# Kernel tuning notes

Hardware: AMD Instinct MI355X
Metric: run time of the kernel (lower is better)

## Reference

```python
import jax, jax.numpy as jnp
import numpy as np

ALPHA = 4.0  # spikingjelly default Sigmoid surrogate alpha
BN_EPS = 1e-5

@jax.custom_vjp
def _spike(v):
    return (v >= 0.0).astype(v.dtype)

def _spike_fwd(v):
    return _spike(v), v

def _spike_bwd(v, g):
    s = jax.nn.sigmoid(ALPHA * v)
    return (g * ALPHA * s * (1.0 - s),)

_spike.defvjp(_spike_fwd, _spike_bwd)

def lif(x, v_th):
    # Single-step LIFNode(tau=2, v_reset=0) starting from v=0:
    # v = v + (x - v)/tau = x/2 ; spike = Heaviside(v - v_th)
    return _spike(x * 0.5 - v_th)

def bn(x, p):
    # p: [4, C] = gamma, beta, running_mean, running_var (inference BN)
    g, b, m, v = p
    scale = g * jax.lax.rsqrt(v + BN_EPS)
    return x * scale[None, :, None, None] + (b - m * scale)[None, :, None, None]

def conv1x1(x, w):
    # x: [B,C,H,W], w: [O,C]
    return jnp.einsum('bchw,oc->bohw', x, w)

def dwconv3x3(x, w):
    # depthwise 3x3, w: [C,3,3]
    C = x.shape[1]
    return jax.lax.conv_general_dilated(
        x, w[:, None], (1, 1), 'SAME',
        feature_group_count=C,
        dimension_numbers=('NCHW', 'OIHW', 'NCHW'))

def branch(x, w1, dw, w2, bns):
    # RepConv: conv1x1 -> BN -> (dw3x3 -> pw1x1 -> BN), then the extra Sequential BN
    x = bn(conv1x1(x, w1), bns[0])
    x = bn(conv1x1(dwconv3x3(x, dw), w2), bns[1])
    return bn(x, bns[2])

def setup_inputs() -> dict:
    key = jax.random.key(0)
    ks = jax.random.split(key, 5)
    B, C, H, W = 16, 256, 80, 80
    x = jax.random.normal(ks[0], (B, C, H, W), jnp.float32) * 2.0  # so LIFs actually fire
    w1 = jax.random.normal(ks[1], (4, C, C), jnp.float32) * 0.06
    dw = jax.random.normal(ks[2], (4, C, 3, 3), jnp.float32) * 0.3
    w2 = jax.random.normal(ks[3], (4, C, C), jnp.float32) * 0.06
    bn_params = jax.random.uniform(ks[4], (4, 3, 4, C), jnp.float32, 0.1, 1.0)
    return {"x": x, "w1": w1, "dw": dw, "w2": w2, "bn_params": bn_params}

def reference(x, w1, dw, w2, bn_params):
    scale = 0.125
    xs = lif(x, 1.0)                                   # head_lif
    q = branch(xs, w1[0], dw[0], w2[0], bn_params[0])  # q_conv (q_lif unused in source)
    k = branch(xs, w1[1], dw[1], w2[1], bn_params[1])  # k_conv (k_lif unused in source)
    v = branch(xs, w1[2], dw[2], w2[2], bn_params[2])  # v_conv
    v = lif(v, 1.0)                                    # v_lif -> binary spikes
    # k.transpose(-2,-1) @ v : per (b,c) [W,H] @ [H,W] -> [W,W]
    kv = jnp.einsum('bchw,bchu->bcwu', k, v)
    # q @ kv : [H,W] @ [W,W] -> [H,W]
    attn = jnp.einsum('bchw,bcwu->bchu', q, kv) * scale
    s = lif(attn, 0.5)                                 # attn_lif, v_threshold=0.5
    return branch(s, w1[3], dw[3], w2[3], bn_params[3])  # proj_conv
```

## Files before the change

### kernel.cpp

```cpp
#include <hip/hip_runtime.h>
#include <hip/hip_bf16.h>
#include <cstdint>
#include <cstddef>
#include <cmath>

typedef unsigned short u16;
typedef unsigned char  u8;
typedef unsigned int   u32;
typedef __attribute__((ext_vector_type(8))) short short8;
typedef __attribute__((ext_vector_type(4))) float f32x4;
typedef __attribute__((ext_vector_type(4))) u16 u16x4;

#define CCH 256
#define HWP 6400

__device__ __forceinline__ u16 f2bf(float f) {
  u32 u = __float_as_uint(f);
  u = (u + 0x7FFFu + ((u >> 16) & 1u)) >> 16;
  return (u16)u;
}
__device__ __forceinline__ float bf2f(u16 h) { return __uint_as_float(((u32)h) << 16); }
__device__ __forceinline__ void split3(float v, u16& h, u16& m, u16& l) {
  h = f2bf(v); float r = v - bf2f(h);
  m = f2bf(r); l = f2bf(r - bf2f(m));
}
__device__ __forceinline__ void gl_lds16(const void* g, void* l) {
  __builtin_amdgcn_global_load_lds((const __attribute__((address_space(1))) unsigned int*)g,
                                   (__attribute__((address_space(3))) unsigned int*)l,
                                   16, 0, 0);
}

__global__ __launch_bounds__(256) void fold_weights(
    const float* __restrict__ w1, const float* __restrict__ w2,
    const float* __restrict__ bnp,
    u16* __restrict__ w1h, u16* __restrict__ w1m, u16* __restrict__ w1l,
    u16* __restrict__ w2h, u16* __restrict__ w2m, u16* __restrict__ w2l,
    float* __restrict__ b0f, float* __restrict__ b2f)
{
  int i = blockIdx.x >> 8, o = blockIdx.x & 255, c = threadIdx.x;
  const float* bp = bnp + i * 3072;
  double g0 = bp[0 + o],    be0 = bp[256 + o],  m0 = bp[512 + o],  v0 = bp[768 + o];
  double g1 = bp[1024 + o], be1 = bp[1280 + o], m1 = bp[1536 + o], v1 = bp[1792 + o];
  double g2 = bp[2048 + o], be2 = bp[2304 + o], m2 = bp[2560 + o], v2 = bp[2816 + o];
  double s0 = g0 / sqrt(v0 + 1e-5);
  double s1 = g1 / sqrt(v1 + 1e-5);
  double s2 = g2 / sqrt(v2 + 1e-5);
  size_t ro = (size_t)(i * 256 + o) * 256;
  float wa = (float)(s0 * (double)w1[ro + c]);
  float wb = (float)(s1 * s2 * (double)w2[ro + c]);
  u16 h, m, l;
  split3(wa, h, m, l); w1h[ro + c] = h; w1m[ro + c] = m; w1l[ro + c] = l;
  split3(wb, h, m, l); w2h[ro + c] = h; w2m[ro + c] = m; w2l[ro + c] = l;
  if (c == 0) {
    b0f[i * 256 + o] = (float)(be0 - m0 * s0);
    b2f[i * 256 + o] = (float)(s2 * (be1 - m1 * s1) + be2 - m2 * s2);
  }
}

__global__ __launch_bounds__(256) void head_spike(
    const float* __restrict__ x, u8* __restrict__ xs, int b0)
{
  __shared__ u8 tile[64][68];
  int z = blockIdx.z, c0 = blockIdx.y << 6, p0 = blockIdx.x << 6;
  int tid = threadIdx.x;
  const float* xb = x + ((size_t)(b0 + z) * CCH + c0) * HWP + p0;
#pragma unroll
  for (int j = 0; j < 16; ++j) {
    int idx = j * 256 + tid;
    int cl = idx >> 6, pl = idx & 63;
    tile[pl][cl] = (xb[(size_t)cl * HWP + pl] >= 2.0f) ? 1 : 0;
  }
  __syncthreads();
#pragma unroll
  for (int j = 0; j < 4; ++j) {
    int idx = j * 256 + tid;
    int row = idx >> 4, c4 = (idx & 15) << 2;
    *(uchar4*)(xs + ((size_t)z * HWP + p0 + row) * CCH + c0 + c4) =
        *(const uchar4*)&tile[row][c4];
  }
}

__global__ __launch_bounds__(256) void transpose_s(
    const u8* __restrict__ in, u8* __restrict__ out, int b0)
{
  __shared__ u8 tile[64][68];
  int z = blockIdx.z, c0 = blockIdx.y << 6, p0 = blockIdx.x << 6;
  int tid = threadIdx.x;
#pragma unroll
  for (int j = 0; j < 4; ++j) {
    int idx = j * 256 + tid;
    int cl = idx >> 4, p4 = (idx & 15) << 2;
    uchar4 v = *(const uchar4*)(in + ((size_t)z * CCH + c0 + cl) * HWP + p0 + p4);
    tile[p4 + 0][cl] = v.x; tile[p4 + 1][cl] = v.y;
    tile[p4 + 2][cl] = v.z; tile[p4 + 3][cl] = v.w;
  }
  __syncthreads();
#pragma unroll
  for (int j = 0; j < 4; ++j) {
    int idx = j * 256 + tid;
    int row = idx >> 4, c4 = (idx & 15) << 2;
    *(uchar4*)(out + ((size_t)(b0 + z) * HWP + p0 + row) * CCH + c0 + c4) =
        *(const uchar4*)&tile[row][c4];
  }
}

__global__ __launch_bounds__(256) void gemm1(
    const u8* __restrict__ act, int b0in,
    const u16* __restrict__ WH, const u16* __restrict__ WM, const u16* __restrict__ WL,
    const float* __restrict__ bias, float* __restrict__ T1)
{
  __shared__ alignas(16) u16 As[128 * 40];
  __shared__ alignas(16) u16 LWH[4096];
  __shared__ alignas(16) u16 LWM[4096];
  __shared__ alignas(16) u16 LWL[4096];
  const int tid = threadIdx.x, wave = tid >> 6, lane = tid & 63;
  const int p0 = blockIdx.x * 128, o0 = blockIdx.y * 128, z = blockIdx.z;
  const int wm = (wave >> 1) * 64, wn = (wave & 1) * 64;
  const int lc = lane & 15, lr = lane >> 4;
  const u8* ab = act + ((size_t)(b0in + z) * HWP + p0) * CCH;
  const char* whb = (const char*)(WH + (size_t)o0 * 256);
  const char* wmb = (const char*)(WM + (size_t)o0 * 256);
  const char* wlb = (const char*)(WL + (size_t)o0 * 256);

  f32x4 acc[4][4];
#pragma unroll
  for (int i = 0; i < 4; ++i)
#pragma unroll
    for (int j = 0; j < 4; ++j) acc[i][j] = (f32x4){0.f, 0.f, 0.f, 0.f};

  const int srow = tid >> 1, shalf = tid & 1;

  for (int kc = 0; kc < 8; ++kc) {
    const int kof = kc * 64;
    __syncthreads();
#pragma unroll
    for (int t = 0; t < 2; ++t) {
      int li = t * 256 + tid;
      int row = li >> 2, ch = li & 3;
      int chp = (ch - row - (row >> 2)) & 3;
      size_t so = (size_t)row * 512 + kof + chp * 16;
      int base = (t * 256 + wave * 64) * 8;
      gl_lds16(whb + so, &LWH[base]);
      gl_lds16(wmb + so, &LWM[base]);
      gl_lds16(wlb + so, &LWL[base]);
    }
    uint4 u = *(const uint4*)(ab + (size_t)srow * CCH + kc * 32 + shalf * 16);
    u32 vv[4] = {u.x, u.y, u.z, u.w};
    u32 w[8];
#pragma unroll
    for (int q = 0; q < 4; ++q) {
      u32 v = vv[q];
      w[2 * q]     = ((v & 255u) ? 0x3F80u : 0u) | (((v >> 8) & 255u) ? 0x3F800000u : 0u);
      w[2 * q + 1] = (((v >> 16) & 255u) ? 0x3F80u : 0u) | (((v >> 24) & 255u) ? 0x3F800000u : 0u);
    }
    *(uint4*)&As[srow * 40 + shalf * 16]     = (uint4){w[0], w[1], w[2], w[3]};
    *(uint4*)&As[srow * 40 + shalf * 16 + 8] = (uint4){w[4], w[5], w[6], w[7]};
    __syncthreads();
    short8 af[4];
#pragma unroll
    for (int i = 0; i < 4; ++i)
      af[i] = *(const short8*)&As[(wm + i * 16 + lc) * 40 + lr * 8];
#pragma unroll
    for (int j = 0; j < 4; ++j) {
      int row = wn + j * 16 + lc;
      int o = row * 32 + ((lr + lc + (lc >> 2)) & 3) * 8;
      short8 bh = *(const short8*)&LWH[o];
      short8 bm = *(const short8*)&LWM[o];
      short8 bl = *(const short8*)&LWL[o];
#pragma unroll
      for (int i = 0; i < 4; ++i) {
        acc[i][j] = __builtin_amdgcn_mfma_f32_16x16x32_bf16(af[i], bl, acc[i][j], 0, 0, 0);
        acc[i][j] = __builtin_amdgcn_mfma_f32_16x16x32_bf16(af[i], bm, acc[i][j], 0, 0, 0);
        acc[i][j] = __builtin_amdgcn_mfma_f32_16x16x32_bf16(af[i], bh, acc[i][j], 0, 0, 0);
      }
    }
  }
  float* tb = T1 + ((size_t)z * HWP + p0) * CCH + o0;
#pragma unroll
  for (int j = 0; j < 4; ++j) {
    int n = wn + j * 16 + lc;
    float bn_ = bias[o0 + n];
#pragma unroll
    for (int i = 0; i < 4; ++i) {
      int m = wm + i * 16 + lr * 4;
#pragma unroll
      for (int r = 0; r < 4; ++r)
        tb[(size_t)(m + r) * CCH + n] = acc[i][j][r] + bn_;
    }
  }
}

__global__ __launch_bounds__(256) void dw3(
    const float* __restrict__ t1, const float* __restrict__ dwk,
    u16* __restrict__ oh, u16* __restrict__ om, u16* __restrict__ ol)
{
  __shared__ float wl[2304];
  int tid = threadIdx.x;
#pragma unroll
  for (int t = 0; t < 9; ++t) wl[t * 256 + tid] = dwk[t * 256 + tid];
  int c4 = (tid & 63) << 2;
  int pl = tid >> 6;
  int p = blockIdx.x * 4 + pl;
  int z = blockIdx.y;
  int y = p / 80, x = p - y * 80;
  __syncthreads();
  float a0 = 0.f, a1 = 0.f, a2 = 0.f, a3 = 0.f;
  const float* base = t1 + (size_t)z * HWP * CCH;
  const float* wc = &wl[c4 * 9];
#pragma unroll
  for (int dy = -1; dy <= 1; ++dy) {
    int yy = y + dy;
    bool vy = (unsigned)yy < 80u;
#pragma unroll
    for (int dx = -1; dx <= 1; ++dx) {
      int xx = x + dx;
      if (vy && (unsigned)xx < 80u) {
        float4 v = *(const float4*)(base + (size_t)(yy * 80 + xx) * CCH + c4);
        int t = (dy + 1) * 3 + (dx + 1);
        a0 += wc[t]      * v.x;
        a1 += wc[9 + t]  * v.y;
        a2 += wc[18 + t] * v.z;
        a3 += wc[27 + t] * v.w;
      }
    }
  }
  u16 h0, m0, l0, h1, m1, l1, h2, m2, l2, h3, m3, l3;
  split3(a0, h0, m0, l0);
  split3(a1, h1, m1, l1);
  split3(a2, h2, m2, l2);
  split3(a3, h3, m3, l3);
  u16x4 vh, vm, vlo;
  vh.x = h0; vh.y = h1; vh.z = h2; vh.w = h3;
  vm.x = m0; vm.y = m1; vm.z = m2; vm.w = m3;
  vlo.x = l0; vlo.y = l1; vlo.z = l2; vlo.w = l3;
  size_t addr = ((size_t)z * HWP + p) * CCH + c4;
  *(u16x4*)(oh + addr) = vh;
  *(u16x4*)(om + addr) = vm;
  *(u16x4*)(ol + addr) = vlo;
}

template <int MODE>
__global__ __launch_bounds__(256) void gemm2s(
    const u16* __restrict__ AH, const u16* __restrict__ AM, const u16* __restrict__ AL,
    const u16* __restrict__ WH, const u16* __restrict__ WM, const u16* __restrict__ WL,
    const float* __restrict__ bias, int b0,
    float* __restrict__ outF, u8* __restrict__ outB)
{
  __shared__ alignas(16) u16 LAH[4096];
  __shared__ alignas(16) u16 LAM[4096];
  __shared__ alignas(16) u16 LAL[4096];
  __shared__ alignas(16) u16 LWH[4096];
  __shared__ alignas(16) u16 LWM[4096];
  __shared__ alignas(16) u16 LWL[4096];
  const int tid = threadIdx.x, wave = tid >> 6, lane = tid & 63;
  const int p0 = blockIdx.x * 128, o0 = blockIdx.y * 128, z = blockIdx.z;
  const int wm = (wave >> 1) * 64, wn = (wave & 1) * 64;
  const int lc = lane & 15, lr = lane >> 4;
  const char* ahb = (const char*)(AH + ((size_t)z * HWP + p0) * 256);
  const char* amb = (const char*)(AM + ((size_t)z * HWP + p0) * 256);
  const char* alb = (const char*)(AL + ((size_t)z * HWP + p0) * 256);
  const char* whb = (const char*)(WH + (size_t)o0 * 256);
  const char* wmb = (const char*)(WM + (size_t)o0 * 256);
  const char* wlb = (const char*)(WL + (size_t)o0 * 256);

  f32x4 acc[4][4];
#pragma unroll
  for (int i = 0; i < 4; ++i)
#pragma unroll
    for (int j = 0; j < 4; ++j) acc[i][j] = (f32x4){0.f, 0.f, 0.f, 0.f};

  for (int kc = 0; kc < 8; ++kc) {
    const int kof = kc * 64;
#pragma unroll
    for (int t = 0; t < 2; ++t) {
      int li = t * 256 + tid;
      int row = li >> 2, ch = li & 3;
      int chp = (ch - row - (row >> 2)) & 3;
      size_t so = (size_t)row * 512 + kof + chp * 16;
      int base = (t * 256 + wave * 64) * 8;
      gl_lds16(ahb + so, &LAH[base]);
      gl_lds16(amb + so, &LAM[base]);
      gl_lds16(alb + so, &LAL[base]);
      gl_lds16(whb + so, &LWH[base]);
      gl_lds16(wmb + so, &LWM[base]);
      gl_lds16(wlb + so, &LWL[base]);
    }
    __syncthreads();
    short8 afH[4], afM[4], afL[4];
#pragma unroll
    for (int i = 0; i < 4; ++i) {
      int row = wm + i * 16 + lc;
      int o = row * 32 + ((lr + lc + (lc >> 2)) & 3) * 8;
      afH[i] = *(const short8*)&LAH[o];
      afM[i] = *(const short8*)&LAM[o];
      afL[i] = *(const short8*)&LAL[o];
    }
#pragma unroll
    for (int j = 0; j < 4; ++j) {
      int row = wn + j * 16 + lc;
      int o = row * 32 + ((lr + lc + (lc >> 2)) & 3) * 8;
      short8 bh = *(const short8*)&LWH[o];
      short8 bm = *(const short8*)&LWM[o];
      short8 bl = *(const short8*)&LWL[o];
#pragma unroll
      for (int i = 0; i < 4; ++i) {
        acc[i][j] = __builtin_amdgcn_mfma_f32_16x16x32_bf16(afM[i], bm, acc[i][j], 0, 0, 0);
        acc[i][j] = __builtin_amdgcn_mfma_f32_16x16x32_bf16(afL[i], bh, acc[i][j], 0, 0, 0);
        acc[i][j] = __builtin_amdgcn_mfma_f32_16x16x32_bf16(afH[i], bl, acc[i][j], 0, 0, 0);
        acc[i][j] = __builtin_amdgcn_mfma_f32_16x16x32_bf16(afM[i], bh, acc[i][j], 0, 0, 0);
        acc[i][j] = __builtin_amdgcn_mfma_f32_16x16x32_bf16(afH[i], bm, acc[i][j], 0, 0, 0);
        acc[i][j] = __builtin_amdgcn_mfma_f32_16x16x32_bf16(afH[i], bh, acc[i][j], 0, 0, 0);
      }
    }
    __syncthreads();
  }
#pragma unroll
  for (int j = 0; j < 4; ++j) {
    int n = o0 + wn + j * 16 + lc;
    float bn_ = bias[n];
    size_t rowb = ((size_t)(b0 + z) * CCH + n) * HWP + p0;
#pragma unroll
    for (int i = 0; i < 4; ++i) {
      int m = wm + i * 16 + lr * 4;
      if (MODE == 0) {
        float4 o;
        o.x = acc[i][j][0] + bn_; o.y = acc[i][j][1] + bn_;
        o.z = acc[i][j][2] + bn_; o.w = acc[i][j][3] + bn_;
        *(float4*)(outF + rowb + m) = o;
      } else {
        uchar4 o;
        o.x = (acc[i][j][0] + bn_ >= 2.0f) ? 1 : 0;
        o.y = (acc[i][j][1] + bn_ >= 2.0f) ? 1 : 0;
        o.z = (acc[i][j][2] + bn_ >= 2.0f) ? 1 : 0;
        o.w = (acc[i][j][3] + bn_ >= 2.0f) ? 1 : 0;
        *(uchar4*)(outB + rowb + m) = o;
      }
    }
  }
}

__global__ __launch_bounds__(320) void attn_k(
    const float* __restrict__ qf, const float* __restrict__ kf,
    const u8* __restrict__ vv, u8* __restrict__ s)
{
  __shared__ alignas(16) u16 L[24960];
  __shared__ alignas(16) u8  VT[8320];
  const int tid = threadIdx.x, wave = tid >> 6, lane = tid & 63;
  const int lc = lane & 15, lr = lane >> 4;
  const size_t off = (size_t)blockIdx.x * HWP;
  u16* KH = L; u16* KM = L + 8320; u16* KL = L + 16640;

  for (int t = 0; t < 12; ++t) {
    int i = t * 320 + tid;
    if (i < 3840) {
      int pl = i / 1280, rem = i - pl * 1280;
      L[pl * 8320 + (rem >> 4) * 104 + 80 + (rem & 15)] = 0;
    }
  }
  for (int t = 0; t < 4; ++t) {
    int i = t * 320 + tid;
    if (i < 1280) VT[(i >> 4) * 104 + 80 + (i & 15)] = 0;
  }
  for (int t = 0; t < 20; ++t) {
    int idx = t * 320 + tid;
    int h = idx / 80, w = idx - h * 80;
    u16 hh, mm, ll; split3(kf[off + idx], hh, mm, ll);
    KH[h * 104 + w] = hh; KM[h * 104 + w] = mm; KL[h * 104 + w] = ll;
    VT[w * 104 + h] = vv[off + idx];
  }
  __syncthreads();

  f32x4 accS[5];
#pragma unroll
  for (int n = 0; n < 5; ++n) accS[n] = (f32x4){0.f, 0.f, 0.f, 0.f};
  const int hrow = wave * 16 + lc;
  for (int kc = 0; kc < 3; ++kc) {
    short8 qh, qm, ql;
    int w0 = kc * 32 + lr * 8;
    if (w0 < 80) {
      const float* qp = qf + off + hrow * 80 + w0;
      float4 a = *(const float4*)qp;
      float4 b = *(const float4*)(qp + 4);
      float qv[8] = {a.x, a.y, a.z, a.w, b.x, b.y, b.z, b.w};
#pragma unroll
      for (int e = 0; e < 8; ++e) {
        u16 hh, mm, ll; split3(qv[e], hh, mm, ll);
        qh[e] = (short)hh; qm[e] = (short)mm; ql[e] = (short)ll;
      }
    } else {
      qh = (short8){0,0,0,0,0,0,0,0}; qm = qh; ql = qh;
    }
#pragma unroll
    for (int n = 0; n < 5; ++n) {
      int bo = (n * 16 + lc) * 104 + kc * 32 + lr * 8;
      short8 kh_ = *(const short8*)&KH[bo];
      short8 km_ = *(const short8*)&KM[bo];
      short8 kl_ = *(const short8*)&KL[bo];
      accS[n] = __builtin_amdgcn_mfma_f32_16x16x32_bf16(qh, kl_, accS[n], 0, 0, 0);
      accS[n] = __builtin_amdgcn_mfma_f32_16x16x32_bf16(ql, kh_, accS[n], 0, 0, 0);
      accS[n] = __builtin_amdgcn_mfma_f32_16x16x32_bf16(qm, km_, accS[n], 0, 0, 0);
      accS[n] = __builtin_amdgcn_mfma_f32_16x16x32_bf16(qm, kh_, accS[n], 0, 0, 0);
      accS[n] = __builtin_amdgcn_mfma_f32_16x16x32_bf16(qh, km_, accS[n], 0, 0, 0);
      accS[n] = __builtin_amdgcn_mfma_f32_16x16x32_bf16(qh, kh_, accS[n], 0, 0, 0);
    }
  }
  __syncthreads();
  for (int t = 0; t < 12; ++t) {
    int i = t * 320 + tid;
    if (i < 3840) {
      int pl = i / 1280, rem = i - pl * 1280;
      L[pl * 8320 + (rem >> 4) * 104 + 80 + (rem & 15)] = 0;
    }
  }
#pragma unroll
  for (int n = 0; n < 5; ++n) {
#pragma unroll
    for (int r = 0; r < 4; ++r) {
      u16 hh, mm, ll; split3(accS[n][r], hh, mm, ll);
      int o = (wave * 16 + lr * 4 + r) * 104 + n * 16 + lc;
      KH[o] = hh; KM[o] = mm; KL[o] = ll;
    }
  }
  __syncthreads();
  f32x4 accA[5];
#pragma unroll
  for (int n = 0; n < 5; ++n) accA[n] = (f32x4){0.f, 0.f, 0.f, 0.f};
  for (int kc = 0; kc < 3; ++kc) {
    int ao = (wave * 16 + lc) * 104 + kc * 32 + lr * 8;
    short8 sh_ = *(const short8*)&KH[ao];
    short8 sm_ = *(const short8*)&KM[ao];
    short8 sl_ = *(const short8*)&KL[ao];
#pragma unroll
    for (int n = 0; n < 5; ++n) {
      const u8* vp = &VT[(n * 16 + lc) * 104 + kc * 32 + lr * 8];
      u32 b0 = *(const u32*)vp;
      u32 b1 = *(const u32*)(vp + 4);
      u32 e0 = ((b0 & 255u) ? 0x3F80u : 0u) | (((b0 >> 8) & 255u) ? 0x3F800000u : 0u);
      u32 e1 = (((b0 >> 16) & 255u) ? 0x3F80u : 0u) | (((b0 >> 24) & 255u) ? 0x3F800000u : 0u);
      u32 e2 = ((b1 & 255u) ? 0x3F80u : 0u) | (((b1 >> 8) & 255u) ? 0x3F800000u : 0u);
      u32 e3 = (((b1 >> 16) & 255u) ? 0x3F80u : 0u) | (((b1 >> 24) & 255u) ? 0x3F800000u : 0u);
      u32 vbw[4] = {e0, e1, e2, e3};
      short8 vb = *(const short8*)vbw;
      accA[n] = __builtin_amdgcn_mfma_f32_16x16x32_bf16(sl_, vb, accA[n], 0, 0, 0);
      accA[n] = __builtin_amdgcn_mfma_f32_16x16x32_bf16(sm_, vb, accA[n], 0, 0, 0);
      accA[n] = __builtin_amdgcn_mfma_f32_16x16x32_bf16(sh_, vb, accA[n], 0, 0, 0);
    }
  }
#pragma unroll
  for (int n = 0; n < 5; ++n)
#pragma unroll
    for (int r = 0; r < 4; ++r)
      s[off + (size_t)(wave * 16 + lr * 4 + r) * 80 + n * 16 + lc] =
          (accA[n][r] >= 8.0f) ? 1 : 0;
}

extern "C" void kernel_launch(void* const* d_in, const int* in_sizes, int n_in,
                              void* d_out, int out_size, void* d_ws, size_t ws_size,
                              hipStream_t stream)
{
  const float* x   = (const float*)d_in[0];
  const float* w1  = (const float*)d_in[1];
  const float* dwk = (const float*)d_in[2];
  const float* w2  = (const float*)d_in[3];
  const float* bnp = (const float*)d_in[4];
  float* out = (float*)d_out;
  char* ws = (char*)d_ws;

  u16* W1H = (u16*)(ws + 0);
  u16* W1M = (u16*)(ws + 524288);
  u16* W1L = (u16*)(ws + 1048576);
  u16* W2H = (u16*)(ws + 1572864);
  u16* W2M = (u16*)(ws + 2097152);
  u16* W2L = (u16*)(ws + 2621440);
  float* B0F = (float*)(ws + 3145728);
  float* B2F = (float*)(ws + 3149824);
  u8*    SPM = (u8*)(ws + 3153920);
  u8*    XS  = (u8*)(ws + 29368320);
  float* T1  = (float*)(ws + 42475520);
  float* QF  = (float*)(ws + 94904320);
  float* KF  = (float*)(ws + 147333120);
  u8*    V   = (u8*)(ws + 199761920);
  u16*   D2H = (u16*)(ws + 212869120);
  u16*   D2M = (u16*)(ws + 239083520);
  u16*   D2L = (u16*)(ws + 265297920);

  dim3 gb(256);
  fold_weights<<<dim3(1024), gb, 0, stream>>>(w1, w2, bnp,
      W1H, W1M, W1L, W2H, W2M, W2L, B0F, B2F);

  for (int c = 0; c < 2; ++c) {
    int b0 = c * 8;
    dim3 gh(100, 4, 8), gg(50, 2, 8), gd(1600, 8);
    head_spike<<<gh, gb, 0, stream>>>(x, XS, b0);
    gemm1<<<gg, gb, 0, stream>>>(XS, 0, W1H + 0 * 65536, W1M + 0 * 65536, W1L + 0 * 65536,
                                 B0F + 0, T1);
    dw3<<<gd, gb, 0, stream>>>(T1, dwk + 0 * 2304, D2H, D2M, D2L);
    gemm2s<0><<<gg, gb, 0, stream>>>(D2H, D2M, D2L,
                                     W2H + 0 * 65536, W2M + 0 * 65536, W2L + 0 * 65536,
                                     B2F + 0, 0, QF, nullptr);
    gemm1<<<gg, gb, 0, stream>>>(XS, 0, W1H + 1 * 65536, W1M + 1 * 65536, W1L + 1 * 65536,
                                 B0F + 256, T1);
    dw3<<<gd, gb, 0, stream>>>(T1, dwk + 1 * 2304, D2H, D2M, D2L);
    gemm2s<0><<<gg, gb, 0, stream>>>(D2H, D2M, D2L,
                                     W2H + 1 * 65536, W2M + 1 * 65536, W2L + 1 * 65536,
                                     B2F + 256, 0, KF, nullptr);
    gemm1<<<gg, gb, 0, stream>>>(XS, 0, W1H + 2 * 65536, W1M + 2 * 65536, W1L + 2 * 65536,
                                 B0F + 512, T1);
    dw3<<<gd, gb, 0, stream>>>(T1, dwk + 2 * 2304, D2H, D2M, D2L);
    gemm2s<1><<<gg, gb, 0, stream>>>(D2H, D2M, D2L,
                                     W2H + 2 * 65536, W2M + 2 * 65536, W2L + 2 * 65536,
                                     B2F + 512, 0, nullptr, V);
    attn_k<<<dim3(2048), dim3(320), 0, stream>>>(QF, KF, V, V);
    transpose_s<<<gh, gb, 0, stream>>>(V, SPM, b0);
  }
  for (int c = 0; c < 2; ++c) {
    int b0 = c * 8;
    dim3 gg(50, 2, 8), gd(1600, 8);
    gemm1<<<gg, gb, 0, stream>>>(SPM, b0, W1H + 3 * 65536, W1M + 3 * 65536, W1L + 3 * 65536,
                                 B0F + 768, T1);
    dw3<<<gd, gb, 0, stream>>>(T1, dwk + 3 * 2304, D2H, D2M, D2L);
    gemm2s<0><<<gg, gb, 0, stream>>>(D2H, D2M, D2L,
                                     W2H + 3 * 65536, W2M + 3 * 65536, W2L + 3 * 65536,
                                     B2F + 768, b0, out, nullptr);
  }
}
```

Measured before the change: 1.406 ms.

## Emit split-bf16 Q/K from GEMM epilogue and vectorize attention loads

The second pointwise GEMM for q and k now writes the three-way bf16 split (high/mid/low) directly in its epilogue, so the attention kernel no longer reads fp32 Q/K and re-splits them. The attention kernel loads K with 16-byte vector copies into LDS, loads V with uchar4, and drops the redundant padding re-zeroing. MFMA sequences are wrapped in s_setprio. The branch order changes so v is computed first, which lets K reuse the T1 workspace region. The cost is 1.5x more bytes written and read for Q/K (three u16 planes instead of one float), plus the split arithmetic moved into the GEMM epilogue.

```diff
diff --git a/kernel.cpp b/kernel.cpp
--- a/kernel.cpp
+++ b/kernel.cpp
@@ -244,7 +244,8 @@
     const u16* __restrict__ AH, const u16* __restrict__ AM, const u16* __restrict__ AL,
     const u16* __restrict__ WH, const u16* __restrict__ WM, const u16* __restrict__ WL,
     const float* __restrict__ bias, int b0,
-    float* __restrict__ outF, u8* __restrict__ outB)
+    float* __restrict__ outF, u8* __restrict__ outB,
+    u16* __restrict__ outH, u16* __restrict__ outM, u16* __restrict__ outL)
 {
   __shared__ alignas(16) u16 LAH[4096];
   __shared__ alignas(16) u16 LAM[4096];
@@ -327,20 +328,32 @@
         o.x = acc[i][j][0] + bn_; o.y = acc[i][j][1] + bn_;
         o.z = acc[i][j][2] + bn_; o.w = acc[i][j][3] + bn_;
         *(float4*)(outF + rowb + m) = o;
-      } else {
+      } else if (MODE == 1) {
         uchar4 o;
         o.x = (acc[i][j][0] + bn_ >= 2.0f) ? 1 : 0;
         o.y = (acc[i][j][1] + bn_ >= 2.0f) ? 1 : 0;
         o.z = (acc[i][j][2] + bn_ >= 2.0f) ? 1 : 0;
         o.w = (acc[i][j][3] + bn_ >= 2.0f) ? 1 : 0;
         *(uchar4*)(outB + rowb + m) = o;
+      } else {
+        u16x4 vh, vm2, vl2;
+#pragma unroll
+        for (int r = 0; r < 4; ++r) {
+          u16 hh, mm, ll;
+          split3(acc[i][j][r] + bn_, hh, mm, ll);
+          vh[r] = hh; vm2[r] = mm; vl2[r] = ll;
+        }
+        *(u16x4*)(outH + rowb + m) = vh;
+        *(u16x4*)(outM + rowb + m) = vm2;
+        *(u16x4*)(outL + rowb + m) = vl2;
       }
     }
   }
 }
 
 __global__ __launch_bounds__(320) void attn_k(
-    const float* __restrict__ qf, const float* __restrict__ kf,
+    const u16* __restrict__ qh_g, const u16* __restrict__ qm_g, const u16* __restrict__ ql_g,
+    const u16* __restrict__ kh_g, const u16* __restrict__ km_g, const u16* __restrict__ kl_g,
     const u8* __restrict__ vv, u8* __restrict__ s)
 {
   __shared__ alignas(16) u16 L[24960];
@@ -350,68 +363,75 @@
   const size_t off = (size_t)blockIdx.x * HWP;
   u16* KH = L; u16* KM = L + 8320; u16* KL = L + 16640;
 
-  for (int t = 0; t < 12; ++t) {
-    int i = t * 320 + tid;
-    if (i < 3840) {
-      int pl = i / 1280, rem = i - pl * 1280;
-      L[pl * 8320 + (rem >> 4) * 104 + 80 + (rem & 15)] = 0;
-    }
-  }
-  for (int t = 0; t < 4; ++t) {
-    int i = t * 320 + tid;
-    if (i < 1280) VT[(i >> 4) * 104 + 80 + (i & 15)] = 0;
-  }
-  for (int t = 0; t < 20; ++t) {
-    int idx = t * 320 + tid;
-    int h = idx / 80, w = idx - h * 80;
-    u16 hh, mm, ll; split3(kf[off + idx], hh, mm, ll);
-    KH[h * 104 + w] = hh; KM[h * 104 + w] = mm; KL[h * 104 + w] = ll;
-    VT[w * 104 + h] = vv[off + idx];
-  }
-  __syncthreads();
-
-  f32x4 accS[5];
-#pragma unroll
-  for (int n = 0; n < 5; ++n) accS[n] = (f32x4){0.f, 0.f, 0.f, 0.f};
+  short8 qfr[3][3];
   const int hrow = wave * 16 + lc;
+#pragma unroll
   for (int kc = 0; kc < 3; ++kc) {
-    short8 qh, qm, ql;
     int w0 = kc * 32 + lr * 8;
     if (w0 < 80) {
-      const float* qp = qf + off + hrow * 80 + w0;
-      float4 a = *(const float4*)qp;
-      float4 b = *(const float4*)(qp + 4);
-      float qv[8] = {a.x, a.y, a.z, a.w, b.x, b.y, b.z, b.w};
-#pragma unroll
-      for (int e = 0; e < 8; ++e) {
-        u16 hh, mm, ll; split3(qv[e], hh, mm, ll);
-        qh[e] = (short)hh; qm[e] = (short)mm; ql[e] = (short)ll;
-      }
+      size_t qo = off + (size_t)hrow * 80 + w0;
+      qfr[kc][0] = *(const short8*)(qh_g + qo);
+      qfr[kc][1] = *(const short8*)(qm_g + qo);
+      qfr[kc][2] = *(const short8*)(ql_g + qo);
     } else {
-      qh = (short8){0,0,0,0,0,0,0,0}; qm = qh; ql = qh;
-    }
+      qfr[kc][0] = (short8){0, 0, 0, 0, 0, 0, 0, 0};
+      qfr[kc][1] = qfr[kc][0];
+      qfr[kc][2] = qfr[kc][0];
+    }
+  }
+
+#pragma unroll
+  for (int t = 0; t < 3; ++t) {
+    int g = t * 320 + tid;
+    int h = g / 12, wc = g - h * 12;
+    int dst = h * 104 + wc * 8;
+    if (wc < 10) {
+      size_t so = off + (size_t)h * 80 + wc * 8;
+      *(short8*)&KH[dst] = *(const short8*)(kh_g + so);
+      *(short8*)&KM[dst] = *(const short8*)(km_g + so);
+      *(short8*)&KL[dst] = *(const short8*)(kl_g + so);
+    } else {
+      short8 z8 = (short8){0, 0, 0, 0, 0, 0, 0, 0};
+      *(short8*)&KH[dst] = z8; *(short8*)&KM[dst] = z8; *(short8*)&KL[dst] = z8;
+    }
+  }
+  {
+    int row = tid >> 2, qq = tid & 3;
+    *(u32*)&VT[row * 104 + 80 + qq * 4] = 0;
+  }
+#pragma unroll
+  for (int t = 0; t < 5; ++t) {
+    int q = t * 320 + tid;
+    int h = q / 20, w4 = (q - h * 20) * 4;
+    uchar4 v4 = *(const uchar4*)(vv + off + (size_t)h * 80 + w4);
+    VT[(w4 + 0) * 104 + h] = v4.x;
+    VT[(w4 + 1) * 104 + h] = v4.y;
+    VT[(w4 + 2) * 104 + h] = v4.z;
+    VT[(w4 + 3) * 104 + h] = v4.w;
+  }
+  __syncthreads();
+
+  f32x4 accS[5];
+#pragma unroll
+  for (int n = 0; n < 5; ++n) accS[n] = (f32x4){0.f, 0.f, 0.f, 0.f};
+  for (int kc = 0; kc < 3; ++kc) {
 #pragma unroll
     for (int n = 0; n < 5; ++n) {
       int bo = (n * 16 + lc) * 104 + kc * 32 + lr * 8;
       short8 kh_ = *(const short8*)&KH[bo];
       short8 km_ = *(const short8*)&KM[bo];
       short8 kl_ = *(const short8*)&KL[bo];
-      accS[n] = __builtin_amdgcn_mfma_f32_16x16x32_bf16(qh, kl_, accS[n], 0, 0, 0);
-      accS[n] = __builtin_amdgcn_mfma_f32_16x16x32_bf16(ql, kh_, accS[n], 0, 0, 0);
-      accS[n] = __builtin_amdgcn_mfma_f32_16x16x32_bf16(qm, km_, accS[n], 0, 0, 0);
-      accS[n] = __builtin_amdgcn_mfma_f32_16x16x32_bf16(qm, kh_, accS[n], 0, 0, 0);
-      accS[n] = __builtin_amdgcn_mfma_f32_16x16x32_bf16(qh, km_, accS[n], 0, 0, 0);
-      accS[n] = __builtin_amdgcn_mfma_f32_16x16x32_bf16(qh, kh_, accS[n], 0, 0, 0);
+      __builtin_amdgcn_s_setprio(1);
+      accS[n] = __builtin_amdgcn_mfma_f32_16x16x32_bf16(qfr[kc][0], kl_, accS[n], 0, 0, 0);
+      accS[n] = __builtin_amdgcn_mfma_f32_16x16x32_bf16(qfr[kc][2], kh_, accS[n], 0, 0, 0);
+      accS[n] = __builtin_amdgcn_mfma_f32_16x16x32_bf16(qfr[kc][1], km_, accS[n], 0, 0, 0);
+      accS[n] = __builtin_amdgcn_mfma_f32_16x16x32_bf16(qfr[kc][1], kh_, accS[n], 0, 0, 0);
+      accS[n] = __builtin_amdgcn_mfma_f32_16x16x32_bf16(qfr[kc][0], km_, accS[n], 0, 0, 0);
+      accS[n] = __builtin_amdgcn_mfma_f32_16x16x32_bf16(qfr[kc][0], kh_, accS[n], 0, 0, 0);
+      __builtin_amdgcn_s_setprio(0);
     }
   }
   __syncthreads();
-  for (int t = 0; t < 12; ++t) {
-    int i = t * 320 + tid;
-    if (i < 3840) {
-      int pl = i / 1280, rem = i - pl * 1280;
-      L[pl * 8320 + (rem >> 4) * 104 + 80 + (rem & 15)] = 0;
-    }
-  }
 #pragma unroll
   for (int n = 0; n < 5; ++n) {
 #pragma unroll
@@ -441,9 +461,11 @@
       u32 e3 = (((b1 >> 16) & 255u) ? 0x3F80u : 0u) | (((b1 >> 24) & 255u) ? 0x3F800000u : 0u);
       u32 vbw[4] = {e0, e1, e2, e3};
       short8 vb = *(const short8*)vbw;
+      __builtin_amdgcn_s_setprio(1);
       accA[n] = __builtin_amdgcn_mfma_f32_16x16x32_bf16(sl_, vb, accA[n], 0, 0, 0);
       accA[n] = __builtin_amdgcn_mfma_f32_16x16x32_bf16(sm_, vb, accA[n], 0, 0, 0);
       accA[n] = __builtin_amdgcn_mfma_f32_16x16x32_bf16(sh_, vb, accA[n], 0, 0, 0);
+      __builtin_amdgcn_s_setprio(0);
     }
   }
 #pragma unroll
@@ -477,8 +499,12 @@
   u8*    SPM = (u8*)(ws + 3153920);
   u8*    XS  = (u8*)(ws + 29368320);
   float* T1  = (float*)(ws + 42475520);
-  float* QF  = (float*)(ws + 94904320);
-  float* KF  = (float*)(ws + 147333120);
+  u16*   KH_ = (u16*)(ws + 42475520);
+  u16*   KM_ = (u16*)(ws + 68689920);
+  u16*   QH_ = (u16*)(ws + 94904320);
+  u16*   QM_ = (u16*)(ws + 121118720);
+  u16*   QL_ = (u16*)(ws + 147333120);
+  u16*   KL_ = (u16*)(ws + 173547520);
   u8*    V   = (u8*)(ws + 199761920);
   u16*   D2H = (u16*)(ws + 212869120);
   u16*   D2M = (u16*)(ws + 239083520);
@@ -492,25 +518,25 @@
     int b0 = c * 8;
     dim3 gh(100, 4, 8), gg(50, 2, 8), gd(1600, 8);
     head_spike<<<gh, gb, 0, stream>>>(x, XS, b0);
-    gemm1<<<gg, gb, 0, stream>>>(XS, 0, W1H + 0 * 65536, W1M + 0 * 65536, W1L + 0 * 65536,
-                                 B0F + 0, T1);
-    dw3<<<gd, gb, 0, stream>>>(T1, dwk + 0 * 2304, D2H, D2M, D2L);
-    gemm2s<0><<<gg, gb, 0, stream>>>(D2H, D2M, D2L,
-                                     W2H + 0 * 65536, W2M + 0 * 65536, W2L + 0 * 65536,
-                                     B2F + 0, 0, QF, nullptr);
-    gemm1<<<gg, gb, 0, stream>>>(XS, 0, W1H + 1 * 65536, W1M + 1 * 65536, W1L + 1 * 65536,
-                                 B0F + 256, T1);
-    dw3<<<gd, gb, 0, stream>>>(T1, dwk + 1 * 2304, D2H, D2M, D2L);
-    gemm2s<0><<<gg, gb, 0, stream>>>(D2H, D2M, D2L,
-                                     W2H + 1 * 65536, W2M + 1 * 65536, W2L + 1 * 65536,
-                                     B2F + 256, 0, KF, nullptr);
     gemm1<<<gg, gb, 0, stream>>>(XS, 0, W1H + 2 * 65536, W1M + 2 * 65536, W1L + 2 * 65536,
                                  B0F + 512, T1);
     dw3<<<gd, gb, 0, stream>>>(T1, dwk + 2 * 2304, D2H, D2M, D2L);
     gemm2s<1><<<gg, gb, 0, stream>>>(D2H, D2M, D2L,
                                      W2H + 2 * 65536, W2M + 2 * 65536, W2L + 2 * 65536,
-                                     B2F + 512, 0, nullptr, V);
-    attn_k<<<dim3(2048), dim3(320), 0, stream>>>(QF, KF, V, V);
+                                     B2F + 512, 0, nullptr, V, nullptr, nullptr, nullptr);
+    gemm1<<<gg, gb, 0, stream>>>(XS, 0, W1H + 0 * 65536, W1M + 0 * 65536, W1L + 0 * 65536,
+                                 B0F + 0, T1);
+    dw3<<<gd, gb, 0, stream>>>(T1, dwk + 0 * 2304, D2H, D2M, D2L);
+    gemm2s<2><<<gg, gb, 0, stream>>>(D2H, D2M, D2L,
+                                     W2H + 0 * 65536, W2M + 0 * 65536, W2L + 0 * 65536,
+                                     B2F + 0, 0, nullptr, nullptr, QH_, QM_, QL_);
+    gemm1<<<gg, gb, 0, stream>>>(XS, 0, W1H + 1 * 65536, W1M + 1 * 65536, W1L + 1 * 65536,
+                                 B0F + 256, T1);
+    dw3<<<gd, gb, 0, stream>>>(T1, dwk + 1 * 2304, D2H, D2M, D2L);
+    gemm2s<2><<<gg, gb, 0, stream>>>(D2H, D2M, D2L,
+                                     W2H + 1 * 65536, W2M + 1 * 65536, W2L + 1 * 65536,
+                                     B2F + 256, 0, nullptr, nullptr, KH_, KM_, KL_);
+    attn_k<<<dim3(2048), dim3(320), 0, stream>>>(QH_, QM_, QL_, KH_, KM_, KL_, V, V);
     transpose_s<<<gh, gb, 0, stream>>>(V, SPM, b0);
   }
   for (int c = 0; c < 2; ++c) {
@@ -521,6 +547,6 @@
     dw3<<<gd, gb, 0, stream>>>(T1, dwk + 3 * 2304, D2H, D2M, D2L);
     gemm2s<0><<<gg, gb, 0, stream>>>(D2H, D2M, D2L,
                                      W2H + 3 * 65536, W2M + 3 * 65536, W2L + 3 * 65536,
-                                     B2F + 768, b0, out, nullptr);
-  }
-}
+                                     B2F + 768, b0, out, nullptr, nullptr, nullptr, nullptr);
+  }
+}
```

After: 1.438 ms. 2.2% more time.
